# Kernel optimization log

Hardware: AMD Instinct MI355X
Metric: run time of the kernel (lower is better)

The kernel has to match this reference:

```python
import jax, jax.numpy as jnp
import numpy as np
from jax import lax

INPUT_DIM = 12
T = 2048
H = 512
L = 6
EPS = 1e-5


def setup_inputs() -> dict:
    key = jax.random.key(0)
    ks = jax.random.split(key, 12)
    s = 1.0 / np.sqrt(H)
    inp = {
        "x": jax.random.normal(ks[0], (32, INPUT_DIM), dtype=jnp.float32),
        "in_proj_w": jax.random.normal(ks[1], (H, INPUT_DIM), dtype=jnp.float32) * (1.0 / np.sqrt(INPUT_DIM)),
        "in_proj_b": jnp.zeros((H,), dtype=jnp.float32),
        "W_ih": jax.random.uniform(ks[2], (L, 4 * H, H), dtype=jnp.float32, minval=-s, maxval=s),
        "W_hh": jax.random.uniform(ks[3], (L, 4 * H, H), dtype=jnp.float32, minval=-s, maxval=s),
        "b_ih": jax.random.uniform(ks[4], (L, 4 * H), dtype=jnp.float32, minval=-s, maxval=s),
        "b_hh": jax.random.uniform(ks[5], (L, 4 * H), dtype=jnp.float32, minval=-s, maxval=s),
        "ln_scale": jnp.ones((L, H), dtype=jnp.float32),
        "ln_bias": jnp.zeros((L, H), dtype=jnp.float32),
        "out_w": jax.random.normal(ks[6], (1, H), dtype=jnp.float32) * s,
        "out_b": jnp.zeros((1,), dtype=jnp.float32),
    }
    return inp


def _lstm_layer(h_in, Wih, Whh, bih, bhh):
    # h_in: (B, T, H); PyTorch gate order: i, f, g, o
    B = h_in.shape[0]
    xg = jnp.einsum("bth,gh->btg", h_in, Wih) + bih  # (B, T, 4H) input gates precomputed
    xg_t = jnp.swapaxes(xg, 0, 1)  # (T, B, 4H)
    h0 = jnp.zeros((B, H), dtype=h_in.dtype)
    c0 = jnp.zeros((B, H), dtype=h_in.dtype)

    def step(carry, xt):
        h, c = carry
        gates = xt + h @ Whh.T + bhh
        i, f, g, o = jnp.split(gates, 4, axis=-1)
        i = jax.nn.sigmoid(i)
        f = jax.nn.sigmoid(f)
        g = jnp.tanh(g)
        o = jax.nn.sigmoid(o)
        c = f * c + i * g
        h = o * jnp.tanh(c)
        return (h, c), h

    _, hs = lax.scan(step, (h0, c0), xg_t)  # hs: (T, B, H)
    return jnp.swapaxes(hs, 0, 1)


def _layernorm(x, scale, bias):
    mu = jnp.mean(x, axis=-1, keepdims=True)
    var = jnp.mean(jnp.square(x - mu), axis=-1, keepdims=True)
    return (x - mu) * lax.rsqrt(var + EPS) * scale + bias


def reference(x, in_proj_w, in_proj_b, W_ih, W_hh, b_ih, b_hh, ln_scale, ln_bias, out_w, out_b):
    x_proj = x @ in_proj_w.T + in_proj_b  # (B, H)
    h = jnp.broadcast_to(x_proj[:, None, :], (x.shape[0], T, H))  # repeat along time
    for l in range(L):
        out = _lstm_layer(h, W_ih[l], W_hh[l], b_ih[l], b_hh[l])
        h = _layernorm(out + h, ln_scale[l], ln_bias[l])  # dropout = identity (eval)
    y = jnp.einsum("bth,oh->bto", h, out_w) + out_b  # (B, T, 1)
    return y[..., 0]  # (B, T)
```

## Files before the change

kernel.cpp:

```cpp
#include <hip/hip_runtime.h>

#define NS 2058

typedef __attribute__((ext_vector_type(4))) int   i32x4;
typedef __attribute__((ext_vector_type(8))) short s16x8;
typedef __attribute__((ext_vector_type(4))) float f32x4;

__device__ __forceinline__ unsigned short f2bf(float f) {
  unsigned u = __float_as_uint(f);
  unsigned r = u + 0x7FFFu + ((u >> 16) & 1u);
  return (unsigned short)(r >> 16);
}
__device__ __forceinline__ unsigned pack2bf(float lo, float hi) {
  return (unsigned)f2bf(lo) | ((unsigned)f2bf(hi) << 16);
}
__device__ __forceinline__ float bflo(unsigned u){ return __uint_as_float(u << 16); }
__device__ __forceinline__ float bfhi(unsigned u){ return __uint_as_float(u & 0xFFFF0000u); }

__device__ __forceinline__ float sigm(float x){ return 1.0f / (1.0f + __expf(-x)); }
__device__ __forceinline__ float tanh_(float x){
  float ax = fabsf(x);
  float e  = __expf(-2.0f * ax);
  float t  = (1.0f - e) / (1.0f + e);
  return copysignf(t, x);
}

__global__ __launch_bounds__(256) void k_inproj(const float* __restrict__ x,
                                                const float* __restrict__ w,
                                                const float* __restrict__ bb,
                                                float* __restrict__ XP) {
  int idx = blockIdx.x * 256 + threadIdx.x;
  int b = idx >> 9, j = idx & 511;
  float acc = bb[j];
#pragma unroll
  for (int k = 0; k < 12; ++k) acc += x[b * 12 + k] * w[j * 12 + k];
  XP[idx] = acc;
}

__global__ __launch_bounds__(256) void k_xg0(const float* __restrict__ XP,
                                             const float* __restrict__ Wih,
                                             const float* __restrict__ bih,
                                             float* __restrict__ XG0) {
  int idx = blockIdx.x * 256 + threadIdx.x;
  int b = idx & 31;
  int r = idx >> 5;
  const float* wr = Wih + (size_t)r * 512;
  const float* xr = XP + b * 512;
  float acc = bih[r];
  for (int k = 0; k < 512; k += 4) {
    const f32x4 w4 = *(const f32x4*)(wr + k);
    const f32x4 x4 = *(const f32x4*)(xr + k);
    acc += w4[0]*x4[0] + w4[1]*x4[1] + w4[2]*x4[2] + w4[3]*x4[3];
  }
  XG0[b * 2048 + r] = acc;
}

__global__ __launch_bounds__(256, 1) void k_pipe(
    const float* __restrict__ Wih, const float* __restrict__ Whh,
    const float* __restrict__ bih, const float* __restrict__ bhh,
    const float* __restrict__ lnS, const float* __restrict__ lnB,
    const float* __restrict__ XG0, const float* __restrict__ XP,
    unsigned* __restrict__ Hst,
    unsigned* __restrict__ Roll,
    unsigned long long* __restrict__ Part,
    unsigned* __restrict__ RB,
    unsigned* __restrict__ flg)
{
  __shared__ char smem[65536];
  char* xarea = smem;
  char* harea = smem + 32768;

  const int tid   = threadIdx.x;
  const int wgid  = blockIdx.x;
  const int layer = wgid >> 5;
  const int w     = wgid & 31;
  const int lane  = tid & 63;
  const int wv    = tid >> 6;
  const int j0    = w << 4;
  float* gacc = (float*)(layer == 0 ? (smem + 10240) : smem);

  unsigned* HstL = Hst + layer * 16384;

  s16x8 bfih[16], bfhh[16];
  {
    const int rcol = lane & 15;
    const int kg   = lane >> 4;
    const size_t rowbase = ((size_t)layer * 2048 + (size_t)(wv * 512 + j0 + rcol)) * 512;
    const float* ihr = Wih + rowbase;
    const float* hhr = Whh + rowbase;
#pragma unroll
    for (int kk = 0; kk < 16; ++kk) {
      const int k0 = kg * 8 + kk * 32;
      s16x8 v2;
#pragma unroll
      for (int j = 0; j < 8; ++j) v2[j] = (short)f2bf(hhr[k0 + j]);
      bfhh[kk] = v2;
      if (layer > 0) {
        s16x8 v1;
#pragma unroll
        for (int j = 0; j < 8; ++j) v1[j] = (short)f2bf(ihr[k0 + j]);
        bfih[kk] = v1;
      }
    }
  }

  const int ub = tid >> 3;
  const int jp = tid & 7;
  const int kpglob = (j0 >> 1) + jp;

  float bs[4][2];
#pragma unroll
  for (int g = 0; g < 4; ++g)
#pragma unroll
    for (int c = 0; c < 2; ++c) {
      const size_t r = (size_t)layer * 2048 + g * 512 + j0 + 2 * jp + c;
      float vv = bhh[r];
      if (layer > 0) vv += bih[r];
      bs[g][c] = vv;
    }

  float sc0 = 0.f, sc1v = 0.f, bi0 = 0.f, bi1 = 0.f;
  if (layer > 0) {
    sc0  = lnS[(layer - 1) * 512 + 2 * tid];
    sc1v = lnS[(layer - 1) * 512 + 2 * tid + 1];
    bi0  = lnB[(layer - 1) * 512 + 2 * tid];
    bi1  = lnB[(layer - 1) * 512 + 2 * tid + 1];
  }

  if (layer == 0) {
    float* xg0s = (float*)smem;
    float* xps  = (float*)(smem + 8192);
    for (int i = tid; i < 2048; i += 256) {
      int g = i >> 9, b = (i >> 4) & 31, jl = i & 15;
      xg0s[i] = XG0[b * 2048 + g * 512 + j0 + jl];
    }
    for (int i = tid; i < 512; i += 256) {
      int b = i >> 4, jl = i & 15;
      xps[i] = XP[b * 512 + j0 + jl];
    }
  }

  __hip_atomic_store(&HstL[(ub << 8) + kpglob], 0u, __ATOMIC_RELAXED, __HIP_MEMORY_SCOPE_AGENT);

  __syncthreads();
  if (tid == 0)
    __hip_atomic_store(flg + wgid, 1u, __ATOMIC_RELEASE, __HIP_MEMORY_SCOPE_AGENT);
  if (tid < 192) {
    for (;;) {
      unsigned v = __hip_atomic_load(flg + tid, __ATOMIC_RELAXED, __HIP_MEMORY_SCOPE_AGENT);
      if (__all((int)(v >= 1u))) break;
      __builtin_amdgcn_s_sleep(2);
    }
  }
  __syncthreads();

  float xinc0 = 0.f, xinc1 = 0.f;
  if (layer == 0) {
    const float* xps = (const float*)(smem + 8192);
    xinc0 = xps[ub * 16 + 2 * jp];
    xinc1 = xps[ub * 16 + 2 * jp + 1];
  }

  const int rA  = lane & 15;
  const int kg2 = lane >> 4;
  const int swz = (rA & 7) << 4;
  const int ab0 = rA * 1024 + kg2 * 16;
  const int ab1 = ab0 + 16384;

  float creg0 = 0.f, creg1 = 0.f;
  const int tbase = -2 * layer;

#pragma unroll 1
  for (int s = 0; s < NS; ++s) {
    const int t = s + tbase;

    if (0 <= t && t < 2048) {
      unsigned long long hreg[16];
      const unsigned long long* hs = (const unsigned long long*)(HstL + ((t & 1) << 13));
#pragma unroll
      for (int it = 0; it < 16; ++it)
        hreg[it] = __hip_atomic_load(hs + it * 256 + tid, __ATOMIC_RELAXED, __HIP_MEMORY_SCOPE_AGENT);

      float xin0, xin1;
      f32x4 ai0 = {0.f,0.f,0.f,0.f}, ai1 = {0.f,0.f,0.f,0.f};
      if (layer > 0) {
        const unsigned xu = *(const unsigned*)(xarea + (((ub * 1024) + kpglob * 4) ^ ((ub & 7) << 4)));
        xin0 = bflo(xu); xin1 = bfhi(xu);
#pragma unroll
        for (int kk = 0; kk < 16; ++kk) {
          const i32x4 x0 = *(const i32x4*)(xarea + ((ab0 + kk * 64) ^ swz));
          const i32x4 x1 = *(const i32x4*)(xarea + ((ab1 + kk * 64) ^ swz));
          ai0 = __builtin_amdgcn_mfma_f32_16x16x32_bf16(__builtin_bit_cast(s16x8, x0), bfih[kk], ai0, 0, 0, 0);
          ai1 = __builtin_amdgcn_mfma_f32_16x16x32_bf16(__builtin_bit_cast(s16x8, x1), bfih[kk], ai1, 0, 0, 0);
        }
      } else { xin0 = xinc0; xin1 = xinc1; }

#pragma unroll
      for (int it = 0; it < 16; ++it) {
        const int flat = it * 256 + tid;
        const int q = flat >> 7, kp2 = flat & 127;
        *(unsigned long long*)(harea + ((q * 1024 + kp2 * 8) ^ ((q & 7) << 4))) = hreg[it];
      }
      __syncthreads();

      f32x4 acc0, acc1;
      if (layer > 0) {
        f32x4 ah0 = {0.f,0.f,0.f,0.f}, ah1 = {0.f,0.f,0.f,0.f};
#pragma unroll
        for (int kk = 0; kk < 16; ++kk) {
          const i32x4 h0 = *(const i32x4*)(harea + ((ab0 + kk * 64) ^ swz));
          const i32x4 h1 = *(const i32x4*)(harea + ((ab1 + kk * 64) ^ swz));
          ah0 = __builtin_amdgcn_mfma_f32_16x16x32_bf16(__builtin_bit_cast(s16x8, h0), bfhh[kk], ah0, 0, 0, 0);
          ah1 = __builtin_amdgcn_mfma_f32_16x16x32_bf16(__builtin_bit_cast(s16x8, h1), bfhh[kk], ah1, 0, 0, 0);
        }
        acc0 = ai0 + ah0; acc1 = ai1 + ah1;
      } else {
        f32x4 a0a = {0.f,0.f,0.f,0.f}, a1a = {0.f,0.f,0.f,0.f};
        f32x4 a0b = {0.f,0.f,0.f,0.f}, a1b = {0.f,0.f,0.f,0.f};
#pragma unroll
        for (int kk = 0; kk < 8; ++kk) {
          const i32x4 h0a = *(const i32x4*)(harea + ((ab0 + kk * 64) ^ swz));
          const i32x4 h1a = *(const i32x4*)(harea + ((ab1 + kk * 64) ^ swz));
          const i32x4 h0b = *(const i32x4*)(harea + ((ab0 + (kk + 8) * 64) ^ swz));
          const i32x4 h1b = *(const i32x4*)(harea + ((ab1 + (kk + 8) * 64) ^ swz));
          a0a = __builtin_amdgcn_mfma_f32_16x16x32_bf16(__builtin_bit_cast(s16x8, h0a), bfhh[kk], a0a, 0, 0, 0);
          a1a = __builtin_amdgcn_mfma_f32_16x16x32_bf16(__builtin_bit_cast(s16x8, h1a), bfhh[kk], a1a, 0, 0, 0);
          a0b = __builtin_amdgcn_mfma_f32_16x16x32_bf16(__builtin_bit_cast(s16x8, h0b), bfhh[kk + 8], a0b, 0, 0, 0);
          a1b = __builtin_amdgcn_mfma_f32_16x16x32_bf16(__builtin_bit_cast(s16x8, h1b), bfhh[kk + 8], a1b, 0, 0, 0);
        }
        acc0 = a0a + a0b; acc1 = a1a + a1b;
      }
      __syncthreads();
      {
        float* gp = gacc + (wv * 16 + rA) * 36 + kg2 * 4;
        *(f32x4*)gp        = acc0;
        *(f32x4*)(gp + 16) = acc1;
      }
      __syncthreads();

      float pre[4][2];
#pragma unroll
      for (int g = 0; g < 4; ++g)
#pragma unroll
        for (int c = 0; c < 2; ++c) {
          float vv = gacc[(g * 16 + 2 * jp + c) * 36 + ub] + bs[g][c];
          if (layer == 0) vv += ((const float*)smem)[(g * 32 + ub) * 16 + 2 * jp + c];
          pre[g][c] = vv;
        }

      float i0 = sigm(pre[0][0]), ff0 = sigm(pre[1][0]), g0 = tanh_(pre[2][0]), o0 = sigm(pre[3][0]);
      creg0 = ff0 * creg0 + i0 * g0;
      float h0 = o0 * tanh_(creg0);
      float i1 = sigm(pre[0][1]), ff1 = sigm(pre[1][1]), g1 = tanh_(pre[2][1]), o1 = sigm(pre[3][1]);
      creg1 = ff1 * creg1 + i1 * g1;
      float h1 = o1 * tanh_(creg1);
      const float out0 = h0 + xin0, out1 = h1 + xin1;

      if (layer < 5) {
        float sP  = out0 + out1;
        float ssP = out0 * out0 + out1 * out1;
#pragma unroll
        for (int m = 1; m < 8; m <<= 1) { sP += __shfl_xor(sP, m, 64); ssP += __shfl_xor(ssP, m, 64); }
        __hip_atomic_store(&Roll[layer * 32768 + (t & 3) * 8192 + ub * 256 + kpglob],
                           pack2bf(out0, out1), __ATOMIC_RELAXED, __HIP_MEMORY_SCOPE_AGENT);
        if (jp == 0) {
          unsigned long long pp = (unsigned long long)__float_as_uint(sP) |
                                  ((unsigned long long)__float_as_uint(ssP) << 32);
          __hip_atomic_store(&Part[layer * 4096 + (t & 3) * 1024 + w * 32 + ub],
                             pp, __ATOMIC_RELAXED, __HIP_MEMORY_SCOPE_AGENT);
        }
      } else {
        RB[((size_t)ub * 2048 + t) * 256 + kpglob] = pack2bf(out0, out1);
      }
      __hip_atomic_store(&HstL[(((t + 1) & 1) << 13) + (ub << 8) + kpglob], pack2bf(h0, h1),
                         __ATOMIC_RELAXED, __HIP_MEMORY_SCOPE_AGENT);
    }

    __syncthreads();
    if (tid == 0)
      __hip_atomic_store(flg + wgid, (unsigned)(s + 2), __ATOMIC_RELEASE, __HIP_MEMORY_SCOPE_AGENT);
    if (s == NS - 1) break;

    const int r = s + 1 + tbase;
    if (layer > 0 && 0 <= r && r < 2048) {
      const unsigned* RollC = Roll + (layer - 1) * 32768 + (r & 3) * 8192;
      unsigned xreg[32];
#pragma unroll
      for (int q = 0; q < 32; ++q)
        xreg[q] = __hip_atomic_load(RollC + q * 256 + tid, __ATOMIC_RELAXED, __HIP_MEMORY_SCOPE_AGENT);

      const unsigned long long* PartC = Part + (layer - 1) * 4096 + (r & 3) * 1024;
      {
        const int b = tid & 31, w8 = tid >> 5;
        float s4 = 0.f, ss4 = 0.f;
#pragma unroll
        for (int k = 0; k < 4; ++k) {
          unsigned long long pp = __hip_atomic_load(PartC + (w8 + 8 * k) * 32 + b,
                                                    __ATOMIC_RELAXED, __HIP_MEMORY_SCOPE_AGENT);
          s4  += __uint_as_float((unsigned)pp);
          ss4 += __uint_as_float((unsigned)(pp >> 32));
        }
        float* scr = (float*)harea;
        scr[(w8 * 32 + b) * 2]     = s4;
        scr[(w8 * 32 + b) * 2 + 1] = ss4;
      }
      __syncthreads();
      float* stats = (float*)(harea + 2048);
      if (tid < 32) {
        const float* scr = (const float*)harea;
        float ssum = 0.f, sssum = 0.f;
#pragma unroll
        for (int k = 0; k < 8; ++k) { ssum += scr[(k * 32 + tid) * 2]; sssum += scr[(k * 32 + tid) * 2 + 1]; }
        const float mu = ssum * (1.f / 512.f);
        float var = sssum * (1.f / 512.f) - mu * mu;
        const float rs = rsqrtf(var + 1e-5f);
        stats[tid * 2]     = mu;
        stats[tid * 2 + 1] = rs;
      }
      __syncthreads();
#pragma unroll
      for (int q = 0; q < 32; ++q) {
        const float mu = stats[q * 2], rs = stats[q * 2 + 1];
        const unsigned u = xreg[q];
        const float a  = (bflo(u) - mu) * rs * sc0  + bi0;
        const float b2 = (bfhi(u) - mu) * rs * sc1v + bi1;
        *(unsigned*)(xarea + ((q * 1024 + tid * 4) ^ ((q & 7) << 4))) = pack2bf(a, b2);
      }
    }

    {
      const unsigned need = (unsigned)(s + 2);
      if (tid < 192) {
        for (;;) {
          unsigned v = __hip_atomic_load(flg + tid, __ATOMIC_RELAXED, __HIP_MEMORY_SCOPE_AGENT);
          if (__all((int)(v >= need))) break;
          __builtin_amdgcn_s_sleep(2);
        }
      }
      __syncthreads();
    }
  }
}

__global__ __launch_bounds__(256) void k_lnout(const unsigned* __restrict__ Rin,
                                               const float* __restrict__ lnS,
                                               const float* __restrict__ lnB,
                                               const float* __restrict__ ow,
                                               const float* __restrict__ ob,
                                               float* __restrict__ y) {
  int row  = blockIdx.x * 4 + (threadIdx.x >> 6);
  int lane = threadIdx.x & 63;
  const i32x4 v = *(const i32x4*)(Rin + (size_t)row * 256 + lane * 4);
  float xv[8];
#pragma unroll
  for (int j = 0; j < 4; ++j) {
    unsigned u = (unsigned)v[j];
    xv[2*j]   = bflo(u);
    xv[2*j+1] = bfhi(u);
  }
  float s = 0.f, s2 = 0.f;
#pragma unroll
  for (int j = 0; j < 8; ++j) { s += xv[j]; s2 += xv[j] * xv[j]; }
#pragma unroll
  for (int m = 1; m < 64; m <<= 1) { s += __shfl_xor(s, m, 64); s2 += __shfl_xor(s2, m, 64); }
  float mu  = s * (1.f / 512.f);
  float var = s2 * (1.f / 512.f) - mu * mu;
  float rs  = rsqrtf(var + 1e-5f);
  const float* Sp = lnS + 5 * 512 + lane * 8;
  const float* Bp = lnB + 5 * 512 + lane * 8;
  const float* wp = ow + lane * 8;
  float acc = 0.f;
#pragma unroll
  for (int j = 0; j < 8; ++j)
    acc += ((xv[j] - mu) * rs * Sp[j] + Bp[j]) * wp[j];
#pragma unroll
  for (int m = 1; m < 64; m <<= 1) acc += __shfl_xor(acc, m, 64);
  if (lane == 0) y[row] = acc + ob[0];
}

extern "C" void kernel_launch(void* const* d_in, const int* in_sizes, int n_in,
                              void* d_out, int out_size, void* d_ws, size_t ws_size,
                              hipStream_t stream) {
  (void)in_sizes; (void)n_in; (void)out_size; (void)ws_size;
  const float* x   = (const float*)d_in[0];
  const float* ipw = (const float*)d_in[1];
  const float* ipb = (const float*)d_in[2];
  const float* Wih = (const float*)d_in[3];
  const float* Whh = (const float*)d_in[4];
  const float* bih = (const float*)d_in[5];
  const float* bhh = (const float*)d_in[6];
  const float* lnS = (const float*)d_in[7];
  const float* lnB = (const float*)d_in[8];
  const float* ow  = (const float*)d_in[9];
  const float* ob  = (const float*)d_in[10];
  float* y = (float*)d_out;

  char* ws = (char*)d_ws;
  unsigned* flg            = (unsigned*)ws;
  float* XP                = (float*)(ws + 4096);
  float* XG0               = (float*)(ws + 69632);
  unsigned* Hst            = (unsigned*)(ws + 331776);
  unsigned* Roll           = (unsigned*)(ws + 724992);
  unsigned long long* Part = (unsigned long long*)(ws + 1380352);
  unsigned* RB             = (unsigned*)(ws + 2097152);

  hipMemsetAsync(flg, 0, 1024, stream);
  k_inproj<<<64, 256, 0, stream>>>(x, ipw, ipb, XP);
  k_xg0<<<256, 256, 0, stream>>>(XP, Wih, bih, XG0);
  k_pipe<<<192, 256, 0, stream>>>(Wih, Whh, bih, bhh, lnS, lnB, XG0, XP,
                                  Hst, Roll, Part, RB, flg);
  k_lnout<<<16384, 256, 0, stream>>>(RB, lnS, lnB, ow, ob, y);
}
```

Baseline: 19.28 ms.

## Replace global per-step barrier with tagged data polling and backpressure counters

Removes the grid-wide flag barrier that ran every time step across all 192 workgroups. Consumers now spin on 64-bit slots that carry a timestep tag in the upper word next to the bf16 data, so each workgroup waits only on the values it actually reads. A per-layer progress counter gives producers backpressure so the ring buffers do not overrun. This doubles the storage traffic for the hidden state and roll buffers, and adds retry loops plus an extra memset of the hidden-state buffer.

```diff
diff --git a/kernel.cpp b/kernel.cpp
--- a/kernel.cpp
+++ b/kernel.cpp
@@ -23,6 +23,13 @@
   float e  = __expf(-2.0f * ax);
   float t  = (1.0f - e) / (1.0f + e);
   return copysignf(t, x);
+}
+
+__device__ __forceinline__ unsigned long long aload(const unsigned long long* p) {
+  return __hip_atomic_load(p, __ATOMIC_RELAXED, __HIP_MEMORY_SCOPE_AGENT);
+}
+__device__ __forceinline__ void astore(unsigned long long* p, unsigned long long v) {
+  __hip_atomic_store(p, v, __ATOMIC_RELAXED, __HIP_MEMORY_SCOPE_AGENT);
 }
 
 __global__ __launch_bounds__(256) void k_inproj(const float* __restrict__ x,
@@ -60,11 +67,12 @@
     const float* __restrict__ bih, const float* __restrict__ bhh,
     const float* __restrict__ lnS, const float* __restrict__ lnB,
     const float* __restrict__ XG0, const float* __restrict__ XP,
-    unsigned* __restrict__ Hst,
-    unsigned* __restrict__ Roll,
-    unsigned long long* __restrict__ Part,
+    unsigned long long* __restrict__ Hst,
+    unsigned long long* __restrict__ Roll,
+    unsigned long long* __restrict__ PartS,
+    unsigned long long* __restrict__ PartQ,
     unsigned* __restrict__ RB,
-    unsigned* __restrict__ flg)
+    unsigned* __restrict__ Prog)
 {
   __shared__ char smem[65536];
   char* xarea = smem;
@@ -77,9 +85,9 @@
   const int lane  = tid & 63;
   const int wv    = tid >> 6;
   const int j0    = w << 4;
-  float* gacc = (float*)(layer == 0 ? (smem + 10240) : smem);
-
-  unsigned* HstL = Hst + layer * 16384;
+  float* gacc = (float*)(layer == 0 ? (smem + 10240) : (harea + 16384));
+
+  unsigned long long* HstL = Hst + layer * 16384;
 
   s16x8 bfih[16], bfhh[16];
   {
@@ -139,19 +147,6 @@
       xps[i] = XP[b * 512 + j0 + jl];
     }
   }
-
-  __hip_atomic_store(&HstL[(ub << 8) + kpglob], 0u, __ATOMIC_RELAXED, __HIP_MEMORY_SCOPE_AGENT);
-
-  __syncthreads();
-  if (tid == 0)
-    __hip_atomic_store(flg + wgid, 1u, __ATOMIC_RELEASE, __HIP_MEMORY_SCOPE_AGENT);
-  if (tid < 192) {
-    for (;;) {
-      unsigned v = __hip_atomic_load(flg + tid, __ATOMIC_RELAXED, __HIP_MEMORY_SCOPE_AGENT);
-      if (__all((int)(v >= 1u))) break;
-      __builtin_amdgcn_s_sleep(2);
-    }
-  }
   __syncthreads();
 
   float xinc0 = 0.f, xinc1 = 0.f;
@@ -168,18 +163,33 @@
   const int ab1 = ab0 + 16384;
 
   float creg0 = 0.f, creg1 = 0.f;
+  unsigned myC = 0;
   const int tbase = -2 * layer;
+  const int lane31 = lane & 31;
 
 #pragma unroll 1
   for (int s = 0; s < NS; ++s) {
     const int t = s + tbase;
-
-    if (0 <= t && t < 2048) {
-      unsigned long long hreg[16];
-      const unsigned long long* hs = (const unsigned long long*)(HstL + ((t & 1) << 13));
-#pragma unroll
-      for (int it = 0; it < 16; ++it)
-        hreg[it] = __hip_atomic_load(hs + it * 256 + tid, __ATOMIC_RELAXED, __HIP_MEMORY_SCOPE_AGENT);
+    const bool act = (0 <= t) && (t < 2048);
+
+    if (act) {
+      if (layer < 5 && t >= 5) {
+        const unsigned need = (unsigned)(t - 4);
+        while (!__all((int)(myC >= need))) {
+          if (myC < need)
+            myC = __hip_atomic_load(Prog + (layer + 1) * 32 + lane31,
+                                    __ATOMIC_RELAXED, __HIP_MEMORY_SCOPE_AGENT);
+          if (!__all((int)(myC >= need))) __builtin_amdgcn_s_sleep(1);
+        }
+      }
+
+      const unsigned long long* hs = HstL + (size_t)(t & 1) * 8192;
+      unsigned long long a[32];
+#pragma unroll
+      for (int it = 0; it < 32; ++it) {
+        const int q = (it + w) & 31;
+        a[it] = aload(hs + q * 256 + tid);
+      }
 
       float xin0, xin1;
       f32x4 ai0 = {0.f,0.f,0.f,0.f}, ai1 = {0.f,0.f,0.f,0.f};
@@ -195,11 +205,23 @@
         }
       } else { xin0 = xinc0; xin1 = xinc1; }
 
-#pragma unroll
-      for (int it = 0; it < 16; ++it) {
-        const int flat = it * 256 + tid;
-        const int q = flat >> 7, kp2 = flat & 127;
-        *(unsigned long long*)(harea + ((q * 1024 + kp2 * 8) ^ ((q & 7) << 4))) = hreg[it];
+      const unsigned tagh = (unsigned)t;
+      for (;;) {
+        bool bad = false;
+#pragma unroll
+        for (int it = 0; it < 32; ++it)
+          if ((unsigned)(a[it] >> 32) != tagh) {
+            const int q = (it + w) & 31;
+            a[it] = aload(hs + q * 256 + tid);
+            bad = true;
+          }
+        if (!bad) break;
+      }
+
+#pragma unroll
+      for (int it = 0; it < 32; ++it) {
+        const int q = (it + w) & 31;
+        *(unsigned*)(harea + ((q * 1024 + tid * 4) ^ ((q & 7) << 4))) = (unsigned)a[it];
       }
       __syncthreads();
 
@@ -255,90 +277,99 @@
       creg1 = ff1 * creg1 + i1 * g1;
       float h1 = o1 * tanh_(creg1);
       const float out0 = h0 + xin0, out1 = h1 + xin1;
+      const unsigned long long tago = ((unsigned long long)(unsigned)(t + 1)) << 32;
 
       if (layer < 5) {
         float sP  = out0 + out1;
         float ssP = out0 * out0 + out1 * out1;
 #pragma unroll
         for (int m = 1; m < 8; m <<= 1) { sP += __shfl_xor(sP, m, 64); ssP += __shfl_xor(ssP, m, 64); }
-        __hip_atomic_store(&Roll[layer * 32768 + (t & 3) * 8192 + ub * 256 + kpglob],
-                           pack2bf(out0, out1), __ATOMIC_RELAXED, __HIP_MEMORY_SCOPE_AGENT);
+        astore(Roll + layer * 32768 + (size_t)(t & 3) * 8192 + ub * 256 + kpglob,
+               tago | pack2bf(out0, out1));
         if (jp == 0) {
-          unsigned long long pp = (unsigned long long)__float_as_uint(sP) |
-                                  ((unsigned long long)__float_as_uint(ssP) << 32);
-          __hip_atomic_store(&Part[layer * 4096 + (t & 3) * 1024 + w * 32 + ub],
-                             pp, __ATOMIC_RELAXED, __HIP_MEMORY_SCOPE_AGENT);
+          const size_t pi = layer * 4096 + (size_t)(t & 3) * 1024 + w * 32 + ub;
+          astore(PartS + pi, tago | __float_as_uint(sP));
+          astore(PartQ + pi, tago | __float_as_uint(ssP));
         }
       } else {
         RB[((size_t)ub * 2048 + t) * 256 + kpglob] = pack2bf(out0, out1);
       }
-      __hip_atomic_store(&HstL[(((t + 1) & 1) << 13) + (ub << 8) + kpglob], pack2bf(h0, h1),
-                         __ATOMIC_RELAXED, __HIP_MEMORY_SCOPE_AGENT);
-    }
-
-    __syncthreads();
-    if (tid == 0)
-      __hip_atomic_store(flg + wgid, (unsigned)(s + 2), __ATOMIC_RELEASE, __HIP_MEMORY_SCOPE_AGENT);
-    if (s == NS - 1) break;
+      astore(HstL + (size_t)((t + 1) & 1) * 8192 + (ub << 8) + kpglob, tago | pack2bf(h0, h1));
+    }
 
     const int r = s + 1 + tbase;
     if (layer > 0 && 0 <= r && r < 2048) {
-      const unsigned* RollC = Roll + (layer - 1) * 32768 + (r & 3) * 8192;
-      unsigned xreg[32];
-#pragma unroll
-      for (int q = 0; q < 32; ++q)
-        xreg[q] = __hip_atomic_load(RollC + q * 256 + tid, __ATOMIC_RELAXED, __HIP_MEMORY_SCOPE_AGENT);
-
-      const unsigned long long* PartC = Part + (layer - 1) * 4096 + (r & 3) * 1024;
-      {
-        const int b = tid & 31, w8 = tid >> 5;
-        float s4 = 0.f, ss4 = 0.f;
+      const unsigned long long* RollC = Roll + (layer - 1) * 32768 + (size_t)(r & 3) * 8192;
+      unsigned long long xr[32];
+#pragma unroll
+      for (int i = 0; i < 32; ++i) {
+        const int q = (i + w) & 31;
+        xr[i] = aload(RollC + q * 256 + tid);
+      }
+      const int b = tid & 31, w8 = tid >> 5;
+      const unsigned long long* PSc = PartS + (layer - 1) * 4096 + (size_t)(r & 3) * 1024;
+      const unsigned long long* PQc = PartQ + (layer - 1) * 4096 + (size_t)(r & 3) * 1024;
+      unsigned long long ps[4], pq[4];
+#pragma unroll
+      for (int k = 0; k < 4; ++k) {
+        ps[k] = aload(PSc + (w8 + 8 * k) * 32 + b);
+        pq[k] = aload(PQc + (w8 + 8 * k) * 32 + b);
+      }
+      const unsigned tagr = (unsigned)(r + 1);
+      for (;;) {
+        bool bad = false;
+#pragma unroll
+        for (int i = 0; i < 32; ++i)
+          if ((unsigned)(xr[i] >> 32) != tagr) {
+            const int q = (i + w) & 31;
+            xr[i] = aload(RollC + q * 256 + tid);
+            bad = true;
+          }
 #pragma unroll
         for (int k = 0; k < 4; ++k) {
-          unsigned long long pp = __hip_atomic_load(PartC + (w8 + 8 * k) * 32 + b,
-                                                    __ATOMIC_RELAXED, __HIP_MEMORY_SCOPE_AGENT);
-          s4  += __uint_as_float((unsigned)pp);
-          ss4 += __uint_as_float((unsigned)(pp >> 32));
-        }
-        float* scr = (float*)harea;
-        scr[(w8 * 32 + b) * 2]     = s4;
-        scr[(w8 * 32 + b) * 2 + 1] = ss4;
-      }
+          if ((unsigned)(ps[k] >> 32) != tagr) { ps[k] = aload(PSc + (w8 + 8 * k) * 32 + b); bad = true; }
+          if ((unsigned)(pq[k] >> 32) != tagr) { pq[k] = aload(PQc + (w8 + 8 * k) * 32 + b); bad = true; }
+        }
+        if (!bad) break;
+      }
+      float s4 = 0.f, ss4 = 0.f;
+#pragma unroll
+      for (int k = 0; k < 4; ++k) {
+        s4  += __uint_as_float((unsigned)ps[k]);
+        ss4 += __uint_as_float((unsigned)pq[k]);
+      }
+      float* scr = (float*)harea;
+      scr[(w8 * 32 + b) * 2]     = s4;
+      scr[(w8 * 32 + b) * 2 + 1] = ss4;
       __syncthreads();
       float* stats = (float*)(harea + 2048);
       if (tid < 32) {
-        const float* scr = (const float*)harea;
+        const float* sc = (const float*)harea;
         float ssum = 0.f, sssum = 0.f;
 #pragma unroll
-        for (int k = 0; k < 8; ++k) { ssum += scr[(k * 32 + tid) * 2]; sssum += scr[(k * 32 + tid) * 2 + 1]; }
+        for (int k = 0; k < 8; ++k) { ssum += sc[(k * 32 + tid) * 2]; sssum += sc[(k * 32 + tid) * 2 + 1]; }
         const float mu = ssum * (1.f / 512.f);
         float var = sssum * (1.f / 512.f) - mu * mu;
-        const float rs = rsqrtf(var + 1e-5f);
         stats[tid * 2]     = mu;
-        stats[tid * 2 + 1] = rs;
+        stats[tid * 2 + 1] = rsqrtf(var + 1e-5f);
       }
       __syncthreads();
 #pragma unroll
-      for (int q = 0; q < 32; ++q) {
+      for (int i = 0; i < 32; ++i) {
+        const int q = (i + w) & 31;
         const float mu = stats[q * 2], rs = stats[q * 2 + 1];
-        const unsigned u = xreg[q];
-        const float a  = (bflo(u) - mu) * rs * sc0  + bi0;
-        const float b2 = (bfhi(u) - mu) * rs * sc1v + bi1;
-        *(unsigned*)(xarea + ((q * 1024 + tid * 4) ^ ((q & 7) << 4))) = pack2bf(a, b2);
-      }
-    }
-
-    {
-      const unsigned need = (unsigned)(s + 2);
-      if (tid < 192) {
-        for (;;) {
-          unsigned v = __hip_atomic_load(flg + tid, __ATOMIC_RELAXED, __HIP_MEMORY_SCOPE_AGENT);
-          if (__all((int)(v >= need))) break;
-          __builtin_amdgcn_s_sleep(2);
-        }
-      }
-      __syncthreads();
-    }
+        const unsigned u = (unsigned)xr[i];
+        const float av = (bflo(u) - mu) * rs * sc0  + bi0;
+        const float bv = (bfhi(u) - mu) * rs * sc1v + bi1;
+        *(unsigned*)(xarea + ((q * 1024 + tid * 4) ^ ((q & 7) << 4))) = pack2bf(av, bv);
+      }
+    }
+
+    if (layer > 0 && act && tid == 0)
+      __hip_atomic_store(Prog + layer * 32 + w, (unsigned)(t + 1),
+                         __ATOMIC_RELAXED, __HIP_MEMORY_SCOPE_AGENT);
+
+    __syncthreads();
   }
 }
 
@@ -396,18 +427,20 @@
   float* y = (float*)d_out;
 
   char* ws = (char*)d_ws;
-  unsigned* flg            = (unsigned*)ws;
-  float* XP                = (float*)(ws + 4096);
-  float* XG0               = (float*)(ws + 69632);
-  unsigned* Hst            = (unsigned*)(ws + 331776);
-  unsigned* Roll           = (unsigned*)(ws + 724992);
-  unsigned long long* Part = (unsigned long long*)(ws + 1380352);
-  unsigned* RB             = (unsigned*)(ws + 2097152);
-
-  hipMemsetAsync(flg, 0, 1024, stream);
+  unsigned* Prog            = (unsigned*)ws;
+  float* XP                 = (float*)(ws + 4096);
+  float* XG0                = (float*)(ws + 69632);
+  unsigned long long* Hst   = (unsigned long long*)(ws + 331776);
+  unsigned long long* Roll  = (unsigned long long*)(ws + 1118208);
+  unsigned long long* PartS = (unsigned long long*)(ws + 2428928);
+  unsigned long long* PartQ = (unsigned long long*)(ws + 2592768);
+  unsigned* RB              = (unsigned*)(ws + 4194304);
+
+  hipMemsetAsync(Prog, 0, 768, stream);
+  hipMemsetAsync(Hst, 0, 786432, stream);
   k_inproj<<<64, 256, 0, stream>>>(x, ipw, ipb, XP);
   k_xg0<<<256, 256, 0, stream>>>(XP, Wih, bih, XG0);
   k_pipe<<<192, 256, 0, stream>>>(Wih, Whh, bih, bhh, lnS, lnB, XG0, XP,
-                                  Hst, Roll, Part, RB, flg);
+                                  Hst, Roll, PartS, PartQ, RB, Prog);
   k_lnout<<<16384, 256, 0, stream>>>(RB, lnS, lnB, ow, ob, y);
 }
```

Result: slower. 19.87 ms (+3.0%).

## Replace global lockstep barrier with per-layer dataflow flags and bounded ring backpressure

Applied to the files above, without the earlier changes.

Drops the grid-wide barrier in which every step waited on all 192 workgroups. Each workgroup now waits only on the 32 peers of its own layer for the recurrent state and on the previous layer's flags for its input, with a progress counter from the next layer limiting how far ahead it can write into the 4-slot ring. Flags are padded to separate 64-byte lines and the layernorm input reload uses 64-bit loads. Letting layers drift apart should cut barrier latency and skew, but the new multi-party handshakes add risk of deadlock or ring-overwrite ordering bugs.

```diff
diff --git a/kernel.cpp b/kernel.cpp
--- a/kernel.cpp
+++ b/kernel.cpp
@@ -1,6 +1,4 @@
 #include <hip/hip_runtime.h>
-
-#define NS 2058
 
 typedef __attribute__((ext_vector_type(4))) int   i32x4;
 typedef __attribute__((ext_vector_type(8))) short s16x8;
@@ -23,6 +21,25 @@
   float e  = __expf(-2.0f * ax);
   float t  = (1.0f - e) / (1.0f + e);
   return copysignf(t, x);
+}
+
+__device__ __forceinline__ unsigned long long aload(const unsigned long long* p) {
+  return __hip_atomic_load(p, __ATOMIC_RELAXED, __HIP_MEMORY_SCOPE_AGENT);
+}
+__device__ __forceinline__ void astore32(unsigned* p, unsigned v) {
+  __hip_atomic_store(p, v, __ATOMIC_RELAXED, __HIP_MEMORY_SCOPE_AGENT);
+}
+__device__ __forceinline__ void astore64(unsigned long long* p, unsigned long long v) {
+  __hip_atomic_store(p, v, __ATOMIC_RELAXED, __HIP_MEMORY_SCOPE_AGENT);
+}
+
+__device__ __forceinline__ void waitflags(const unsigned* Flg, int base, unsigned need, int lane) {
+  const unsigned* p = Flg + ((base + (lane & 31)) << 4);
+  unsigned v = __hip_atomic_load(p, __ATOMIC_RELAXED, __HIP_MEMORY_SCOPE_AGENT);
+  while (!__all((int)(v >= need))) {
+    __builtin_amdgcn_s_sleep(1);
+    v = __hip_atomic_load(p, __ATOMIC_RELAXED, __HIP_MEMORY_SCOPE_AGENT);
+  }
 }
 
 __global__ __launch_bounds__(256) void k_inproj(const float* __restrict__ x,
@@ -60,26 +77,27 @@
     const float* __restrict__ bih, const float* __restrict__ bhh,
     const float* __restrict__ lnS, const float* __restrict__ lnB,
     const float* __restrict__ XG0, const float* __restrict__ XP,
-    unsigned* __restrict__ Hst,
-    unsigned* __restrict__ Roll,
+    unsigned long long* __restrict__ Hst,
+    unsigned long long* __restrict__ Roll,
     unsigned long long* __restrict__ Part,
     unsigned* __restrict__ RB,
-    unsigned* __restrict__ flg)
+    unsigned* __restrict__ Flg,
+    unsigned* __restrict__ Prog)
 {
   __shared__ char smem[65536];
-  char* xarea = smem;
-  char* harea = smem + 32768;
-
   const int tid   = threadIdx.x;
   const int wgid  = blockIdx.x;
   const int layer = wgid >> 5;
   const int w     = wgid & 31;
-  const int lane  = tid & 63;
-  const int wv    = tid >> 6;
-  const int j0    = w << 4;
-  float* gacc = (float*)(layer == 0 ? (smem + 10240) : smem);
-
-  unsigned* HstL = Hst + layer * 16384;
+
+  char* xarea = smem;
+  char* harea = smem + 32768;
+  const int lane = tid & 63;
+  const int wv   = tid >> 6;
+  const int j0   = w << 4;
+  float* gacc = (float*)(layer == 0 ? (smem + 10240) : (harea + 16384));
+
+  unsigned long long* HstL = Hst + layer * 8192;
 
   s16x8 bfih[16], bfhh[16];
   {
@@ -119,12 +137,11 @@
       bs[g][c] = vv;
     }
 
-  float sc0 = 0.f, sc1v = 0.f, bi0 = 0.f, bi1 = 0.f;
+  float scp[4] = {0,0,0,0}, bip[4] = {0,0,0,0};
   if (layer > 0) {
-    sc0  = lnS[(layer - 1) * 512 + 2 * tid];
-    sc1v = lnS[(layer - 1) * 512 + 2 * tid + 1];
-    bi0  = lnB[(layer - 1) * 512 + 2 * tid];
-    bi1  = lnB[(layer - 1) * 512 + 2 * tid + 1];
+    const int cb = (layer - 1) * 512 + 4 * (tid & 127);
+#pragma unroll
+    for (int j = 0; j < 4; ++j) { scp[j] = lnS[cb + j]; bip[j] = lnB[cb + j]; }
   }
 
   if (layer == 0) {
@@ -140,19 +157,10 @@
     }
   }
 
-  __hip_atomic_store(&HstL[(ub << 8) + kpglob], 0u, __ATOMIC_RELAXED, __HIP_MEMORY_SCOPE_AGENT);
-
+  astore32((unsigned*)HstL + (ub << 8) + kpglob, 0u);
   __syncthreads();
   if (tid == 0)
-    __hip_atomic_store(flg + wgid, 1u, __ATOMIC_RELEASE, __HIP_MEMORY_SCOPE_AGENT);
-  if (tid < 192) {
-    for (;;) {
-      unsigned v = __hip_atomic_load(flg + tid, __ATOMIC_RELAXED, __HIP_MEMORY_SCOPE_AGENT);
-      if (__all((int)(v >= 1u))) break;
-      __builtin_amdgcn_s_sleep(2);
-    }
-  }
-  __syncthreads();
+    __hip_atomic_store(Flg + ((layer * 32 + w) << 4), 1u, __ATOMIC_RELEASE, __HIP_MEMORY_SCOPE_AGENT);
 
   float xinc0 = 0.f, xinc1 = 0.f;
   if (layer == 0) {
@@ -161,6 +169,51 @@
     xinc1 = xps[ub * 16 + 2 * jp + 1];
   }
 
+  const int b31 = tid & 31, w8 = tid >> 5;
+
+  if (layer > 0) {
+    waitflags(Flg, (layer - 1) * 32, 2u, lane);
+    const unsigned long long* RollC = Roll + (layer - 1) * 16384;
+    const unsigned long long* PC    = Part + (layer - 1) * 4096;
+    unsigned long long xr[16], pr[4];
+#pragma unroll
+    for (int it = 0; it < 16; ++it) xr[it] = aload(RollC + it * 256 + tid);
+#pragma unroll
+    for (int k = 0; k < 4; ++k) pr[k] = aload(PC + (w8 + 8 * k) * 32 + b31);
+    float s4 = 0.f, ss4 = 0.f;
+#pragma unroll
+    for (int k = 0; k < 4; ++k) { s4 += __uint_as_float((unsigned)pr[k]); ss4 += __uint_as_float((unsigned)(pr[k] >> 32)); }
+    float* scr = (float*)harea;
+    scr[(w8 * 32 + b31) * 2]     = s4;
+    scr[(w8 * 32 + b31) * 2 + 1] = ss4;
+    __syncthreads();
+    float* stats = (float*)(harea + 2048);
+    if (tid < 32) {
+      const float* sc = (const float*)harea;
+      float ssum = 0.f, sssum = 0.f;
+#pragma unroll
+      for (int k = 0; k < 8; ++k) { ssum += sc[(k * 32 + tid) * 2]; sssum += sc[(k * 32 + tid) * 2 + 1]; }
+      const float mu = ssum * (1.f / 512.f);
+      float var = sssum * (1.f / 512.f) - mu * mu;
+      stats[tid * 2] = mu; stats[tid * 2 + 1] = rsqrtf(var + 1e-5f);
+    }
+    __syncthreads();
+#pragma unroll
+    for (int it = 0; it < 16; ++it) {
+      const int flat = it * 256 + tid;
+      const int q = flat >> 7, c0 = (flat & 127) * 2;
+      const float mu = stats[q * 2], rs = stats[q * 2 + 1];
+      const unsigned lo = (unsigned)xr[it], hi = (unsigned)(xr[it] >> 32);
+      const float a0 = (bflo(lo) - mu) * rs * scp[0] + bip[0];
+      const float a1 = (bfhi(lo) - mu) * rs * scp[1] + bip[1];
+      const float a2 = (bflo(hi) - mu) * rs * scp[2] + bip[2];
+      const float a3 = (bfhi(hi) - mu) * rs * scp[3] + bip[3];
+      *(unsigned long long*)(xarea + ((q * 1024 + c0 * 4) ^ ((q & 7) << 4))) =
+          (unsigned long long)pack2bf(a0, a1) | ((unsigned long long)pack2bf(a2, a3) << 32);
+    }
+  }
+  __syncthreads();
+
   const int rA  = lane & 15;
   const int kg2 = lane >> 4;
   const int swz = (rA & 7) << 4;
@@ -168,177 +221,171 @@
   const int ab1 = ab0 + 16384;
 
   float creg0 = 0.f, creg1 = 0.f;
-  const int tbase = -2 * layer;
+  unsigned myC = 0;
+  const int lane31 = lane & 31;
 
 #pragma unroll 1
-  for (int s = 0; s < NS; ++s) {
-    const int t = s + tbase;
-
-    if (0 <= t && t < 2048) {
-      unsigned long long hreg[16];
-      const unsigned long long* hs = (const unsigned long long*)(HstL + ((t & 1) << 13));
-#pragma unroll
-      for (int it = 0; it < 16; ++it)
-        hreg[it] = __hip_atomic_load(hs + it * 256 + tid, __ATOMIC_RELAXED, __HIP_MEMORY_SCOPE_AGENT);
-
-      float xin0, xin1;
-      f32x4 ai0 = {0.f,0.f,0.f,0.f}, ai1 = {0.f,0.f,0.f,0.f};
-      if (layer > 0) {
-        const unsigned xu = *(const unsigned*)(xarea + (((ub * 1024) + kpglob * 4) ^ ((ub & 7) << 4)));
-        xin0 = bflo(xu); xin1 = bfhi(xu);
-#pragma unroll
-        for (int kk = 0; kk < 16; ++kk) {
-          const i32x4 x0 = *(const i32x4*)(xarea + ((ab0 + kk * 64) ^ swz));
-          const i32x4 x1 = *(const i32x4*)(xarea + ((ab1 + kk * 64) ^ swz));
-          ai0 = __builtin_amdgcn_mfma_f32_16x16x32_bf16(__builtin_bit_cast(s16x8, x0), bfih[kk], ai0, 0, 0, 0);
-          ai1 = __builtin_amdgcn_mfma_f32_16x16x32_bf16(__builtin_bit_cast(s16x8, x1), bfih[kk], ai1, 0, 0, 0);
-        }
-      } else { xin0 = xinc0; xin1 = xinc1; }
-
-#pragma unroll
-      for (int it = 0; it < 16; ++it) {
-        const int flat = it * 256 + tid;
-        const int q = flat >> 7, kp2 = flat & 127;
-        *(unsigned long long*)(harea + ((q * 1024 + kp2 * 8) ^ ((q & 7) << 4))) = hreg[it];
-      }
-      __syncthreads();
-
-      f32x4 acc0, acc1;
-      if (layer > 0) {
-        f32x4 ah0 = {0.f,0.f,0.f,0.f}, ah1 = {0.f,0.f,0.f,0.f};
-#pragma unroll
-        for (int kk = 0; kk < 16; ++kk) {
-          const i32x4 h0 = *(const i32x4*)(harea + ((ab0 + kk * 64) ^ swz));
-          const i32x4 h1 = *(const i32x4*)(harea + ((ab1 + kk * 64) ^ swz));
-          ah0 = __builtin_amdgcn_mfma_f32_16x16x32_bf16(__builtin_bit_cast(s16x8, h0), bfhh[kk], ah0, 0, 0, 0);
-          ah1 = __builtin_amdgcn_mfma_f32_16x16x32_bf16(__builtin_bit_cast(s16x8, h1), bfhh[kk], ah1, 0, 0, 0);
-        }
-        acc0 = ai0 + ah0; acc1 = ai1 + ah1;
-      } else {
-        f32x4 a0a = {0.f,0.f,0.f,0.f}, a1a = {0.f,0.f,0.f,0.f};
-        f32x4 a0b = {0.f,0.f,0.f,0.f}, a1b = {0.f,0.f,0.f,0.f};
-#pragma unroll
-        for (int kk = 0; kk < 8; ++kk) {
-          const i32x4 h0a = *(const i32x4*)(harea + ((ab0 + kk * 64) ^ swz));
-          const i32x4 h1a = *(const i32x4*)(harea + ((ab1 + kk * 64) ^ swz));
-          const i32x4 h0b = *(const i32x4*)(harea + ((ab0 + (kk + 8) * 64) ^ swz));
-          const i32x4 h1b = *(const i32x4*)(harea + ((ab1 + (kk + 8) * 64) ^ swz));
-          a0a = __builtin_amdgcn_mfma_f32_16x16x32_bf16(__builtin_bit_cast(s16x8, h0a), bfhh[kk], a0a, 0, 0, 0);
-          a1a = __builtin_amdgcn_mfma_f32_16x16x32_bf16(__builtin_bit_cast(s16x8, h1a), bfhh[kk], a1a, 0, 0, 0);
-          a0b = __builtin_amdgcn_mfma_f32_16x16x32_bf16(__builtin_bit_cast(s16x8, h0b), bfhh[kk + 8], a0b, 0, 0, 0);
-          a1b = __builtin_amdgcn_mfma_f32_16x16x32_bf16(__builtin_bit_cast(s16x8, h1b), bfhh[kk + 8], a1b, 0, 0, 0);
-        }
-        acc0 = a0a + a0b; acc1 = a1a + a1b;
-      }
-      __syncthreads();
-      {
-        float* gp = gacc + (wv * 16 + rA) * 36 + kg2 * 4;
-        *(f32x4*)gp        = acc0;
-        *(f32x4*)(gp + 16) = acc1;
-      }
-      __syncthreads();
-
-      float pre[4][2];
-#pragma unroll
-      for (int g = 0; g < 4; ++g)
-#pragma unroll
-        for (int c = 0; c < 2; ++c) {
-          float vv = gacc[(g * 16 + 2 * jp + c) * 36 + ub] + bs[g][c];
-          if (layer == 0) vv += ((const float*)smem)[(g * 32 + ub) * 16 + 2 * jp + c];
-          pre[g][c] = vv;
-        }
-
-      float i0 = sigm(pre[0][0]), ff0 = sigm(pre[1][0]), g0 = tanh_(pre[2][0]), o0 = sigm(pre[3][0]);
-      creg0 = ff0 * creg0 + i0 * g0;
-      float h0 = o0 * tanh_(creg0);
-      float i1 = sigm(pre[0][1]), ff1 = sigm(pre[1][1]), g1 = tanh_(pre[2][1]), o1 = sigm(pre[3][1]);
-      creg1 = ff1 * creg1 + i1 * g1;
-      float h1 = o1 * tanh_(creg1);
-      const float out0 = h0 + xin0, out1 = h1 + xin1;
-
-      if (layer < 5) {
-        float sP  = out0 + out1;
-        float ssP = out0 * out0 + out1 * out1;
-#pragma unroll
-        for (int m = 1; m < 8; m <<= 1) { sP += __shfl_xor(sP, m, 64); ssP += __shfl_xor(ssP, m, 64); }
-        __hip_atomic_store(&Roll[layer * 32768 + (t & 3) * 8192 + ub * 256 + kpglob],
-                           pack2bf(out0, out1), __ATOMIC_RELAXED, __HIP_MEMORY_SCOPE_AGENT);
-        if (jp == 0) {
-          unsigned long long pp = (unsigned long long)__float_as_uint(sP) |
-                                  ((unsigned long long)__float_as_uint(ssP) << 32);
-          __hip_atomic_store(&Part[layer * 4096 + (t & 3) * 1024 + w * 32 + ub],
-                             pp, __ATOMIC_RELAXED, __HIP_MEMORY_SCOPE_AGENT);
-        }
-      } else {
-        RB[((size_t)ub * 2048 + t) * 256 + kpglob] = pack2bf(out0, out1);
-      }
-      __hip_atomic_store(&HstL[(((t + 1) & 1) << 13) + (ub << 8) + kpglob], pack2bf(h0, h1),
-                         __ATOMIC_RELAXED, __HIP_MEMORY_SCOPE_AGENT);
-    }
+  for (int t = 0; t < 2048; ++t) {
+    if (layer < 5 && t >= 5) {
+      const unsigned need = (unsigned)(t - 4);
+      while (!__all((int)(myC >= need))) {
+        if (myC < need)
+          myC = __hip_atomic_load(Prog + (((layer + 1) * 32 + lane31) << 4),
+                                  __ATOMIC_RELAXED, __HIP_MEMORY_SCOPE_AGENT);
+        if (!__all((int)(myC >= need))) __builtin_amdgcn_s_sleep(1);
+      }
+    }
+
+    waitflags(Flg, layer * 32, (unsigned)(t + 1), lane);
+
+    const unsigned long long* hs = HstL + (size_t)(t & 1) * 4096;
+    unsigned long long a[16];
+#pragma unroll
+    for (int it = 0; it < 16; ++it)
+      a[it] = aload(hs + it * 256 + tid);
+
+    float xin0, xin1;
+    f32x4 ai0 = {0.f,0.f,0.f,0.f}, ai1 = {0.f,0.f,0.f,0.f};
+    if (layer > 0) {
+      const unsigned xu = *(const unsigned*)(xarea + (((ub * 1024) + kpglob * 4) ^ ((ub & 7) << 4)));
+      xin0 = bflo(xu); xin1 = bfhi(xu);
+#pragma unroll
+      for (int kk = 0; kk < 16; ++kk) {
+        const i32x4 x0 = *(const i32x4*)(xarea + ((ab0 + kk * 64) ^ swz));
+        const i32x4 x1 = *(const i32x4*)(xarea + ((ab1 + kk * 64) ^ swz));
+        ai0 = __builtin_amdgcn_mfma_f32_16x16x32_bf16(__builtin_bit_cast(s16x8, x0), bfih[kk], ai0, 0, 0, 0);
+        ai1 = __builtin_amdgcn_mfma_f32_16x16x32_bf16(__builtin_bit_cast(s16x8, x1), bfih[kk], ai1, 0, 0, 0);
+      }
+    } else { xin0 = xinc0; xin1 = xinc1; }
+
+#pragma unroll
+    for (int it = 0; it < 16; ++it) {
+      const int flat = it * 256 + tid;
+      const int q = flat >> 7, kp2 = flat & 127;
+      *(unsigned long long*)(harea + ((q * 1024 + kp2 * 8) ^ ((q & 7) << 4))) = a[it];
+    }
+    __syncthreads();
+
+    f32x4 acc0, acc1;
+    if (layer > 0) {
+      f32x4 ah0 = {0.f,0.f,0.f,0.f}, ah1 = {0.f,0.f,0.f,0.f};
+#pragma unroll
+      for (int kk = 0; kk < 16; ++kk) {
+        const i32x4 h0 = *(const i32x4*)(harea + ((ab0 + kk * 64) ^ swz));
+        const i32x4 h1 = *(const i32x4*)(harea + ((ab1 + kk * 64) ^ swz));
+        ah0 = __builtin_amdgcn_mfma_f32_16x16x32_bf16(__builtin_bit_cast(s16x8, h0), bfhh[kk], ah0, 0, 0, 0);
+        ah1 = __builtin_amdgcn_mfma_f32_16x16x32_bf16(__builtin_bit_cast(s16x8, h1), bfhh[kk], ah1, 0, 0, 0);
+      }
+      acc0 = ai0 + ah0; acc1 = ai1 + ah1;
+    } else {
+      f32x4 a0a = {0.f,0.f,0.f,0.f}, a1a = {0.f,0.f,0.f,0.f};
+      f32x4 a0b = {0.f,0.f,0.f,0.f}, a1b = {0.f,0.f,0.f,0.f};
+#pragma unroll
+      for (int kk = 0; kk < 8; ++kk) {
+        const i32x4 h0a = *(const i32x4*)(harea + ((ab0 + kk * 64) ^ swz));
+        const i32x4 h1a = *(const i32x4*)(harea + ((ab1 + kk * 64) ^ swz));
+        const i32x4 h0b = *(const i32x4*)(harea + ((ab0 + (kk + 8) * 64) ^ swz));
+        const i32x4 h1b = *(const i32x4*)(harea + ((ab1 + (kk + 8) * 64) ^ swz));
+        a0a = __builtin_amdgcn_mfma_f32_16x16x32_bf16(__builtin_bit_cast(s16x8, h0a), bfhh[kk], a0a, 0, 0, 0);
+        a1a = __builtin_amdgcn_mfma_f32_16x16x32_bf16(__builtin_bit_cast(s16x8, h1a), bfhh[kk], a1a, 0, 0, 0);
+        a0b = __builtin_amdgcn_mfma_f32_16x16x32_bf16(__builtin_bit_cast(s16x8, h0b), bfhh[kk + 8], a0b, 0, 0, 0);
+        a1b = __builtin_amdgcn_mfma_f32_16x16x32_bf16(__builtin_bit_cast(s16x8, h1b), bfhh[kk + 8], a1b, 0, 0, 0);
+      }
+      acc0 = a0a + a0b; acc1 = a1a + a1b;
+    }
+    __syncthreads();
+    {
+      float* gp = gacc + (wv * 16 + rA) * 36 + kg2 * 4;
+      *(f32x4*)gp        = acc0;
+      *(f32x4*)(gp + 16) = acc1;
+    }
+    __syncthreads();
+
+    float pre[4][2];
+#pragma unroll
+    for (int g = 0; g < 4; ++g)
+#pragma unroll
+      for (int c = 0; c < 2; ++c) {
+        float vv = gacc[(g * 16 + 2 * jp + c) * 36 + ub] + bs[g][c];
+        if (layer == 0) vv += ((const float*)smem)[(g * 32 + ub) * 16 + 2 * jp + c];
+        pre[g][c] = vv;
+      }
+
+    float i0 = sigm(pre[0][0]), ff0 = sigm(pre[1][0]), g0 = tanh_(pre[2][0]), o0 = sigm(pre[3][0]);
+    creg0 = ff0 * creg0 + i0 * g0;
+    float h0 = o0 * tanh_(creg0);
+    float i1 = sigm(pre[0][1]), ff1 = sigm(pre[1][1]), g1 = tanh_(pre[2][1]), o1 = sigm(pre[3][1]);
+    creg1 = ff1 * creg1 + i1 * g1;
+    float h1 = o1 * tanh_(creg1);
+    const float out0 = h0 + xin0, out1 = h1 + xin1;
+
+    if (layer < 5) {
+      float sP  = out0 + out1;
+      float ssP = out0 * out0 + out1 * out1;
+#pragma unroll
+      for (int m = 1; m < 8; m <<= 1) { sP += __shfl_xor(sP, m, 64); ssP += __shfl_xor(ssP, m, 64); }
+      astore32((unsigned*)(Roll + layer * 16384 + (size_t)(t & 3) * 4096) + (ub << 8) + kpglob,
+               pack2bf(out0, out1));
+      if (jp == 0)
+        astore64(Part + layer * 4096 + (size_t)(t & 3) * 1024 + w * 32 + ub,
+                 (unsigned long long)__float_as_uint(sP) |
+                 ((unsigned long long)__float_as_uint(ssP) << 32));
+    } else {
+      RB[((size_t)ub * 2048 + t) * 256 + kpglob] = pack2bf(out0, out1);
+    }
+    astore32((unsigned*)(HstL + (size_t)((t + 1) & 1) * 4096) + (ub << 8) + kpglob,
+             pack2bf(h0, h1));
 
     __syncthreads();
     if (tid == 0)
-      __hip_atomic_store(flg + wgid, (unsigned)(s + 2), __ATOMIC_RELEASE, __HIP_MEMORY_SCOPE_AGENT);
-    if (s == NS - 1) break;
-
-    const int r = s + 1 + tbase;
-    if (layer > 0 && 0 <= r && r < 2048) {
-      const unsigned* RollC = Roll + (layer - 1) * 32768 + (r & 3) * 8192;
-      unsigned xreg[32];
-#pragma unroll
-      for (int q = 0; q < 32; ++q)
-        xreg[q] = __hip_atomic_load(RollC + q * 256 + tid, __ATOMIC_RELAXED, __HIP_MEMORY_SCOPE_AGENT);
-
-      const unsigned long long* PartC = Part + (layer - 1) * 4096 + (r & 3) * 1024;
-      {
-        const int b = tid & 31, w8 = tid >> 5;
-        float s4 = 0.f, ss4 = 0.f;
-#pragma unroll
-        for (int k = 0; k < 4; ++k) {
-          unsigned long long pp = __hip_atomic_load(PartC + (w8 + 8 * k) * 32 + b,
-                                                    __ATOMIC_RELAXED, __HIP_MEMORY_SCOPE_AGENT);
-          s4  += __uint_as_float((unsigned)pp);
-          ss4 += __uint_as_float((unsigned)(pp >> 32));
-        }
-        float* scr = (float*)harea;
-        scr[(w8 * 32 + b) * 2]     = s4;
-        scr[(w8 * 32 + b) * 2 + 1] = ss4;
-      }
+      __hip_atomic_store(Flg + ((layer * 32 + w) << 4), (unsigned)(t + 2),
+                         __ATOMIC_RELEASE, __HIP_MEMORY_SCOPE_AGENT);
+
+    if (layer > 0 && t < 2047) {
+      waitflags(Flg, (layer - 1) * 32, (unsigned)(t + 3), lane);
+      const unsigned long long* RollC = Roll + (layer - 1) * 16384 + (size_t)((t + 1) & 3) * 4096;
+      const unsigned long long* PC    = Part + (layer - 1) * 4096 + (size_t)((t + 1) & 3) * 1024;
+      unsigned long long xr[16], pr[4];
+#pragma unroll
+      for (int it = 0; it < 16; ++it) xr[it] = aload(RollC + it * 256 + tid);
+#pragma unroll
+      for (int k = 0; k < 4; ++k) pr[k] = aload(PC + (w8 + 8 * k) * 32 + b31);
+      float s4 = 0.f, ss4 = 0.f;
+#pragma unroll
+      for (int k = 0; k < 4; ++k) { s4 += __uint_as_float((unsigned)pr[k]); ss4 += __uint_as_float((unsigned)(pr[k] >> 32)); }
+      float* scr = (float*)harea;
+      scr[(w8 * 32 + b31) * 2]     = s4;
+      scr[(w8 * 32 + b31) * 2 + 1] = ss4;
       __syncthreads();
       float* stats = (float*)(harea + 2048);
       if (tid < 32) {
-        const float* scr = (const float*)harea;
+        const float* sc = (const float*)harea;
         float ssum = 0.f, sssum = 0.f;
 #pragma unroll
-        for (int k = 0; k < 8; ++k) { ssum += scr[(k * 32 + tid) * 2]; sssum += scr[(k * 32 + tid) * 2 + 1]; }
+        for (int k = 0; k < 8; ++k) { ssum += sc[(k * 32 + tid) * 2]; sssum += sc[(k * 32 + tid) * 2 + 1]; }
         const float mu = ssum * (1.f / 512.f);
         float var = sssum * (1.f / 512.f) - mu * mu;
-        const float rs = rsqrtf(var + 1e-5f);
-        stats[tid * 2]     = mu;
-        stats[tid * 2 + 1] = rs;
+        stats[tid * 2] = mu; stats[tid * 2 + 1] = rsqrtf(var + 1e-5f);
       }
       __syncthreads();
 #pragma unroll
-      for (int q = 0; q < 32; ++q) {
+      for (int it = 0; it < 16; ++it) {
+        const int flat = it * 256 + tid;
+        const int q = flat >> 7, c0 = (flat & 127) * 2;
         const float mu = stats[q * 2], rs = stats[q * 2 + 1];
-        const unsigned u = xreg[q];
-        const float a  = (bflo(u) - mu) * rs * sc0  + bi0;
-        const float b2 = (bfhi(u) - mu) * rs * sc1v + bi1;
-        *(unsigned*)(xarea + ((q * 1024 + tid * 4) ^ ((q & 7) << 4))) = pack2bf(a, b2);
-      }
-    }
-
-    {
-      const unsigned need = (unsigned)(s + 2);
-      if (tid < 192) {
-        for (;;) {
-          unsigned v = __hip_atomic_load(flg + tid, __ATOMIC_RELAXED, __HIP_MEMORY_SCOPE_AGENT);
-          if (__all((int)(v >= need))) break;
-          __builtin_amdgcn_s_sleep(2);
-        }
-      }
-      __syncthreads();
-    }
+        const unsigned lo = (unsigned)xr[it], hi = (unsigned)(xr[it] >> 32);
+        const float a0 = (bflo(lo) - mu) * rs * scp[0] + bip[0];
+        const float a1 = (bfhi(lo) - mu) * rs * scp[1] + bip[1];
+        const float a2 = (bflo(hi) - mu) * rs * scp[2] + bip[2];
+        const float a3 = (bfhi(hi) - mu) * rs * scp[3] + bip[3];
+        *(unsigned long long*)(xarea + ((q * 1024 + c0 * 4) ^ ((q & 7) << 4))) =
+            (unsigned long long)pack2bf(a0, a1) | ((unsigned long long)pack2bf(a2, a3) << 32);
+      }
+      if (tid == 0)
+        astore32(Prog + ((layer * 32 + w) << 4), (unsigned)(t + 1));
+    }
+
+    __syncthreads();
   }
 }
 
@@ -396,18 +443,19 @@
   float* y = (float*)d_out;
 
   char* ws = (char*)d_ws;
-  unsigned* flg            = (unsigned*)ws;
-  float* XP                = (float*)(ws + 4096);
-  float* XG0               = (float*)(ws + 69632);
-  unsigned* Hst            = (unsigned*)(ws + 331776);
-  unsigned* Roll           = (unsigned*)(ws + 724992);
-  unsigned long long* Part = (unsigned long long*)(ws + 1380352);
-  unsigned* RB             = (unsigned*)(ws + 2097152);
-
-  hipMemsetAsync(flg, 0, 1024, stream);
+  unsigned* Flg             = (unsigned*)ws;
+  unsigned* Prog            = (unsigned*)(ws + 16384);
+  float* XP                 = (float*)(ws + 32768);
+  float* XG0                = (float*)(ws + 98304);
+  unsigned long long* Hst   = (unsigned long long*)(ws + 360448);
+  unsigned long long* Roll  = (unsigned long long*)(ws + 753664);
+  unsigned long long* Part  = (unsigned long long*)(ws + 1409024);
+  unsigned* RB              = (unsigned*)(ws + 2097152);
+
+  hipMemsetAsync(ws, 0, 32768, stream);
   k_inproj<<<64, 256, 0, stream>>>(x, ipw, ipb, XP);
   k_xg0<<<256, 256, 0, stream>>>(XP, Wih, bih, XG0);
   k_pipe<<<192, 256, 0, stream>>>(Wih, Whh, bih, bhh, lnS, lnB, XG0, XP,
-                                  Hst, Roll, Part, RB, flg);
+                                  Hst, Roll, Part, RB, Flg, Prog);
   k_lnout<<<16384, 256, 0, stream>>>(RB, lnS, lnB, ow, ob, y);
 }
```

Measured after the change: 18.25 ms. -5.4%, faster.
